# Optimization experiments

Measured on AMD Instinct MI355X. Metric: run time of the kernel, lower is better.

The kernel has to match this reference:

```python
import jax, jax.numpy as jnp
import numpy as np

B, S, H, F, E, TOP_K = 2, 2048, 1024, 2048, 8, 2


def setup_inputs() -> dict:
    key = jax.random.key(0)
    ks = jax.random.split(key, 5)
    scale_h = 1.0 / np.sqrt(H)
    scale_f = 1.0 / np.sqrt(F)
    return {
        "hidden_states": jax.random.normal(ks[0], (B, S, H), jnp.float32),
        "gate_w": jax.random.normal(ks[1], (H, E), jnp.float32) * scale_h,
        "w_up": jax.random.normal(ks[2], (E, H, F), jnp.float32) * scale_h,
        "w_gate": jax.random.normal(ks[3], (E, H, F), jnp.float32) * scale_h,
        "w_down": jax.random.normal(ks[4], (E, F, H), jnp.float32) * scale_f,
    }


def reference(hidden_states, gate_w, w_up, w_gate, w_down):
    b, s, h = hidden_states.shape
    x = hidden_states.reshape(-1, h)                      # [T, H]
    T = x.shape[0]

    # Router: softmax then top-k then renormalize (as in the module)
    router_logits = x @ gate_w                            # [T, E]
    probs = jax.nn.softmax(router_logits, axis=-1)
    routing_weights, selected_experts = jax.lax.top_k(probs, TOP_K)  # [T, K]
    routing_weights = routing_weights / jnp.sum(routing_weights, axis=-1, keepdims=True)
    routing_weights = routing_weights.astype(x.dtype)

    # Per-token combine weight for each expert (sum over k where selected == e).
    # Equals the masked where/+ accumulation in the original (zero where unselected).
    combine = jnp.zeros((T, E), x.dtype).at[
        jnp.arange(T)[:, None], selected_experts
    ].add(routing_weights)                                # [T, E]

    # Dense expert compute on ALL tokens for every expert (faithful to original,
    # where each device runs its expert on the full token set, then psum).
    up = jnp.einsum("th,ehf->etf", x, w_up)               # [E, T, F]
    gate = jnp.einsum("th,ehf->etf", x, w_gate)           # [E, T, F]
    inner = jax.nn.silu(up) * gate                        # note: silu on up_proj, as in source
    expert_out = jnp.einsum("etf,efh->eth", inner, w_down)  # [E, T, H]

    # Weighted combine == psum over expert axis of masked/weighted outputs.
    y = jnp.einsum("te,eth->th", combine, expert_out)     # [T, H]
    return y.reshape(b, s, h)
```

## Files before the change

### kernel.cpp

```cpp
#include <hip/hip_runtime.h>
#include <hip/hip_bf16.h>

typedef __bf16 bf16x8 __attribute__((ext_vector_type(8)));
typedef float f32x4 __attribute__((ext_vector_type(4)));

#define T_TOK 4096
#define H_DIM 1024
#define F_DIM 2048
#define NEXP 8
#define TOTROWS 8192
#define MAXTILES 80

__device__ inline unsigned short f2b(float f) {
    unsigned int u = __float_as_uint(f);
    unsigned int r = (u + 0x7fffu + ((u >> 16) & 1u)) >> 16;
    return (unsigned short)r;
}

__device__ inline void gload16(const void* g, void* l) {
    __builtin_amdgcn_global_load_lds(
        (const __attribute__((address_space(1))) unsigned int*)g,
        (__attribute__((address_space(3))) unsigned int*)l,
        16, 0, 0);
}

__global__ __launch_bounds__(256) void router_kernel(const float* __restrict__ x,
                                                     const float* __restrict__ gw,
                                                     int* __restrict__ sel, float* __restrict__ selw) {
    int t = blockIdx.x * 4 + (threadIdx.x >> 6);
    int lane = threadIdx.x & 63;
    float acc[8] = {0.f,0.f,0.f,0.f,0.f,0.f,0.f,0.f};
    const float* xr = x + (size_t)t * H_DIM;
    for (int h = lane; h < H_DIM; h += 64) {
        float xv = xr[h];
        const float4* g = (const float4*)(gw + h * 8);
        float4 g0 = g[0], g1 = g[1];
        acc[0] += xv * g0.x; acc[1] += xv * g0.y; acc[2] += xv * g0.z; acc[3] += xv * g0.w;
        acc[4] += xv * g1.x; acc[5] += xv * g1.y; acc[6] += xv * g1.z; acc[7] += xv * g1.w;
    }
#pragma unroll
    for (int off = 32; off >= 1; off >>= 1)
#pragma unroll
        for (int e = 0; e < 8; ++e)
            acc[e] += __shfl_down(acc[e], off);
    if (lane == 0) {
        float mx = acc[0];
#pragma unroll
        for (int e = 1; e < 8; ++e) mx = fmaxf(mx, acc[e]);
        float p[8]; float s = 0.f;
#pragma unroll
        for (int e = 0; e < 8; ++e) { p[e] = expf(acc[e] - mx); s += p[e]; }
        float inv_s = 1.f / s;
#pragma unroll
        for (int e = 0; e < 8; ++e) p[e] *= inv_s;
        int e1 = 0; float p1 = p[0];
#pragma unroll
        for (int e = 1; e < 8; ++e) if (p[e] > p1) { p1 = p[e]; e1 = e; }
        int e2 = -1; float p2 = -1.f;
#pragma unroll
        for (int e = 0; e < 8; ++e) { if (e == e1) continue; if (p[e] > p2) { p2 = p[e]; e2 = e; } }
        float inv = 1.f / (p1 + p2);
        sel[t * 2 + 0] = e1; sel[t * 2 + 1] = e2;
        selw[t * 2 + 0] = p1 * inv; selw[t * 2 + 1] = p2 * inv;
    }
}

__global__ __launch_bounds__(256) void scan_kernel(const int* __restrict__ sel,
                                                   int* __restrict__ cnt, int* __restrict__ off,
                                                   int* __restrict__ fill,
                                                   int* __restrict__ tileExp, int* __restrict__ tileM0) {
    __shared__ int h[NEXP];
    int tid = threadIdx.x;
    if (tid < NEXP) h[tid] = 0;
    __syncthreads();
    for (int i = tid; i < TOTROWS; i += 256) atomicAdd(&h[sel[i]], 1);
    __syncthreads();
    if (tid == 0) {
        int o = 0;
        for (int e = 0; e < NEXP; ++e) { cnt[e] = h[e]; off[e] = o; o += h[e]; fill[e] = 0; }
        int nt = 0;
        for (int e = 0; e < NEXP; ++e)
            for (int m0 = 0; m0 < h[e]; m0 += 128) { tileExp[nt] = e; tileM0[nt] = m0; nt++; }
        for (int i = nt; i < MAXTILES; ++i) { tileExp[i] = -1; tileM0[i] = 0; }
    }
}

__global__ __launch_bounds__(256) void scatgath_kernel(const int* __restrict__ sel,
                                                       const float* __restrict__ selw,
                                                       const int* __restrict__ off,
                                                       int* __restrict__ fill,
                                                       float* __restrict__ rowWgt,
                                                       int* __restrict__ tokRow,
                                                       const float* __restrict__ x,
                                                       unsigned short* __restrict__ Xg) {
    __shared__ int rs[2];
    int t = blockIdx.x;
    int tid = threadIdx.x;
    if (tid == 0) {
#pragma unroll
        for (int k = 0; k < 2; ++k) {
            int e = sel[t * 2 + k];
            int slot = atomicAdd(&fill[e], 1);
            int r = off[e] + slot;
            rowWgt[r] = selw[t * 2 + k];
            tokRow[t * 2 + k] = r;
            rs[k] = r;
        }
    }
    __syncthreads();
    int r1 = rs[0], r2 = rs[1];
    float4 v = ((const float4*)(x + (size_t)t * H_DIM))[tid];
    ushort4 o;
    o.x = f2b(v.x); o.y = f2b(v.y); o.z = f2b(v.z); o.w = f2b(v.w);
    ((ushort4*)(Xg + (size_t)r1 * H_DIM))[tid] = o;
    ((ushort4*)(Xg + (size_t)r2 * H_DIM))[tid] = o;
}

__global__ __launch_bounds__(256) void transpose_cvt_kernel(
        const float* __restrict__ w_up, const float* __restrict__ w_gate,
        const float* __restrict__ w_down,
        unsigned short* __restrict__ wTu, unsigned short* __restrict__ wTg,
        unsigned short* __restrict__ wTd) {
    __shared__ unsigned short lt[64 * 68];
    int z = blockIdx.z;
    int e = blockIdx.y;
    const float* src; unsigned short* dst; int R, C, tr, tc;
    if (z == 0)      { src = w_up;   dst = wTu; R = H_DIM; C = F_DIM; }
    else if (z == 1) { src = w_gate; dst = wTg; R = H_DIM; C = F_DIM; }
    else             { src = w_down; dst = wTd; R = F_DIM; C = H_DIM; }
    if (R == H_DIM) { tc = blockIdx.x & 31; tr = blockIdx.x >> 5; }
    else            { tc = blockIdx.x & 15; tr = blockIdx.x >> 4; }
    const float* s = src + (size_t)e * H_DIM * F_DIM;
    unsigned short* d = dst + (size_t)e * H_DIM * F_DIM;
    int r0 = tr * 64, c0 = tc * 64;
    int tid = threadIdx.x;
    int fc = tid & 15, row = tid >> 4;
#pragma unroll
    for (int i = 0; i < 4; ++i) {
        int r = row + i * 16;
        float4 v = *(const float4*)(s + (size_t)(r0 + r) * C + c0 + fc * 4);
        lt[(fc * 4 + 0) * 68 + r] = f2b(v.x);
        lt[(fc * 4 + 1) * 68 + r] = f2b(v.y);
        lt[(fc * 4 + 2) * 68 + r] = f2b(v.z);
        lt[(fc * 4 + 3) * 68 + r] = f2b(v.w);
    }
    __syncthreads();
    int ch = tid & 7, cc = tid >> 3;
#pragma unroll
    for (int i = 0; i < 2; ++i) {
        int c = cc + i * 32;
        uint2 lo = *(const uint2*)&lt[c * 68 + ch * 8];
        uint2 hi = *(const uint2*)&lt[c * 68 + ch * 8 + 4];
        uint4 o = make_uint4(lo.x, lo.y, hi.x, hi.y);
        *(uint4*)(d + (size_t)(c0 + c) * R + r0 + ch * 8) = o;
    }
}

__global__ __launch_bounds__(256, 2) void gemm_upgate_kernel(
        const unsigned short* __restrict__ Xg,
        const unsigned short* __restrict__ wTu,
        const unsigned short* __restrict__ wTg,
        unsigned short* __restrict__ inner,
        const int* __restrict__ tileExp, const int* __restrict__ tileM0,
        const int* __restrict__ off, const int* __restrict__ cnt) {
    __shared__ __align__(16) unsigned short la[128 * 64];
    __shared__ __align__(16) unsigned short lbu[128 * 64];
    __shared__ __align__(16) unsigned short lbg[128 * 64];
    int bt = blockIdx.y;
    int e = tileExp[bt];
    if (e < 0) return;
    int m0 = tileM0[bt];
    int r0 = off[e] + m0;
    int valid = cnt[e] - m0;
    int f0 = blockIdx.x * 128;
    const unsigned short* aB = Xg + (size_t)r0 * H_DIM;
    const unsigned short* bu = wTu + (size_t)e * F_DIM * H_DIM + (size_t)f0 * H_DIM;
    const unsigned short* bg = wTg + (size_t)e * F_DIM * H_DIM + (size_t)f0 * H_DIM;
    int tid = threadIdx.x;
    int lane = tid & 63, wid = tid >> 6;
    int wm = wid >> 1, wn = wid & 1;
    int l16 = lane & 15, quad = lane >> 4;

    int srcOff[4];
#pragma unroll
    for (int it = 0; it < 4; ++it) {
        int chunk = it * 256 + tid;
        int row = chunk >> 3;
        srcOff[it] = row * H_DIM + (((chunk & 7) ^ (row & 7)) << 3);
    }
    f32x4 accU[4][4], accG[4][4];
#pragma unroll
    for (int i = 0; i < 4; ++i)
#pragma unroll
        for (int j = 0; j < 4; ++j) { accU[i][j] = (f32x4)0.f; accG[i][j] = (f32x4)0.f; }

    for (int k0 = 0; k0 < H_DIM; k0 += 64) {
        __syncthreads();
#pragma unroll
        for (int it = 0; it < 4; ++it) {
            int lbase = it * 2048 + wid * 512;
            gload16(aB + srcOff[it] + k0, &la[lbase]);
            gload16(bu + srcOff[it] + k0, &lbu[lbase]);
            gload16(bg + srcOff[it] + k0, &lbg[lbase]);
        }
        __syncthreads();
#pragma unroll
        for (int h = 0; h < 2; ++h) {
            bf16x8 af[4], bfu[4], bfg[4];
#pragma unroll
            for (int i = 0; i < 4; ++i) {
                int lr = wm * 64 + i * 16 + l16;
                af[i] = *(const bf16x8*)&la[lr * 64 + ((((h * 4 + quad) ^ (lr & 7))) << 3)];
            }
#pragma unroll
            for (int j = 0; j < 4; ++j) {
                int lr = wn * 64 + j * 16 + l16;
                int p = lr * 64 + ((((h * 4 + quad) ^ (lr & 7))) << 3);
                bfu[j] = *(const bf16x8*)&lbu[p];
                bfg[j] = *(const bf16x8*)&lbg[p];
            }
#pragma unroll
            for (int i = 0; i < 4; ++i)
#pragma unroll
                for (int j = 0; j < 4; ++j) {
                    accU[i][j] = __builtin_amdgcn_mfma_f32_16x16x32_bf16(af[i], bfu[j], accU[i][j], 0, 0, 0);
                    accG[i][j] = __builtin_amdgcn_mfma_f32_16x16x32_bf16(af[i], bfg[j], accG[i][j], 0, 0, 0);
                }
        }
    }
#pragma unroll
    for (int i = 0; i < 4; ++i) {
#pragma unroll
        for (int rr = 0; rr < 4; ++rr) {
            int ml = wm * 64 + i * 16 + quad * 4 + rr;
            if (ml >= valid) continue;
            size_t base = (size_t)(r0 + ml) * F_DIM + f0;
#pragma unroll
            for (int j = 0; j < 4; ++j) {
                float u = accU[i][j][rr];
                float g = accG[i][j][rr];
                float v = u / (1.f + expf(-u)) * g;
                inner[base + wn * 64 + j * 16 + l16] = f2b(v);
            }
        }
    }
}

__global__ __launch_bounds__(256, 2) void gemm_down_kernel(
        const unsigned short* __restrict__ inner,
        const unsigned short* __restrict__ wTd,
        float* __restrict__ part,
        const int* __restrict__ tileExp, const int* __restrict__ tileM0,
        const int* __restrict__ off, const int* __restrict__ cnt,
        const float* __restrict__ rowWgt) {
    __shared__ __align__(16) unsigned short la[128 * 64];
    __shared__ __align__(16) unsigned short lb[128 * 64];
    int bt = blockIdx.y;
    int e = tileExp[bt];
    if (e < 0) return;
    int m0 = tileM0[bt];
    int r0 = off[e] + m0;
    int valid = cnt[e] - m0;
    int h0 = blockIdx.x * 128;
    const unsigned short* aB = inner + (size_t)r0 * F_DIM;
    const unsigned short* bp = wTd + (size_t)e * H_DIM * F_DIM + (size_t)h0 * F_DIM;
    int tid = threadIdx.x;
    int lane = tid & 63, wid = tid >> 6;
    int wm = wid >> 1, wn = wid & 1;
    int l16 = lane & 15, quad = lane >> 4;

    int srcOff[4];
#pragma unroll
    for (int it = 0; it < 4; ++it) {
        int chunk = it * 256 + tid;
        int row = chunk >> 3;
        srcOff[it] = row * F_DIM + (((chunk & 7) ^ (row & 7)) << 3);
    }
    f32x4 acc[4][4];
#pragma unroll
    for (int i = 0; i < 4; ++i)
#pragma unroll
        for (int j = 0; j < 4; ++j) acc[i][j] = (f32x4)0.f;

    for (int k0 = 0; k0 < F_DIM; k0 += 64) {
        __syncthreads();
#pragma unroll
        for (int it = 0; it < 4; ++it) {
            int lbase = it * 2048 + wid * 512;
            gload16(aB + srcOff[it] + k0, &la[lbase]);
            gload16(bp + srcOff[it] + k0, &lb[lbase]);
        }
        __syncthreads();
#pragma unroll
        for (int h = 0; h < 2; ++h) {
            bf16x8 af[4], bf[4];
#pragma unroll
            for (int i = 0; i < 4; ++i) {
                int lr = wm * 64 + i * 16 + l16;
                af[i] = *(const bf16x8*)&la[lr * 64 + ((((h * 4 + quad) ^ (lr & 7))) << 3)];
            }
#pragma unroll
            for (int j = 0; j < 4; ++j) {
                int lr = wn * 64 + j * 16 + l16;
                bf[j] = *(const bf16x8*)&lb[lr * 64 + ((((h * 4 + quad) ^ (lr & 7))) << 3)];
            }
#pragma unroll
            for (int i = 0; i < 4; ++i)
#pragma unroll
                for (int j = 0; j < 4; ++j)
                    acc[i][j] = __builtin_amdgcn_mfma_f32_16x16x32_bf16(af[i], bf[j], acc[i][j], 0, 0, 0);
        }
    }
#pragma unroll
    for (int i = 0; i < 4; ++i) {
#pragma unroll
        for (int rr = 0; rr < 4; ++rr) {
            int ml = wm * 64 + i * 16 + quad * 4 + rr;
            if (ml >= valid) continue;
            int gr = r0 + ml;
            float w = rowWgt[gr];
            float* orow = part + (size_t)gr * H_DIM + h0;
#pragma unroll
            for (int j = 0; j < 4; ++j)
                orow[wn * 64 + j * 16 + l16] = w * acc[i][j][rr];
        }
    }
}

__global__ __launch_bounds__(256) void combine_kernel(const float* __restrict__ part,
                                                      const int* __restrict__ tokRow,
                                                      float* __restrict__ out) {
    int t = blockIdx.x;
    int r1 = tokRow[t * 2 + 0], r2 = tokRow[t * 2 + 1];
    int i = threadIdx.x;
    float4 a = ((const float4*)(part + (size_t)r1 * H_DIM))[i];
    float4 b = ((const float4*)(part + (size_t)r2 * H_DIM))[i];
    float4 o;
    o.x = a.x + b.x; o.y = a.y + b.y; o.z = a.z + b.z; o.w = a.w + b.w;
    ((float4*)(out + (size_t)t * H_DIM))[i] = o;
}

extern "C" void kernel_launch(void* const* d_in, const int* in_sizes, int n_in,
                              void* d_out, int out_size, void* d_ws, size_t ws_size,
                              hipStream_t stream) {
    const float* x      = (const float*)d_in[0];
    const float* gw     = (const float*)d_in[1];
    const float* w_up   = (const float*)d_in[2];
    const float* w_gate = (const float*)d_in[3];
    const float* w_down = (const float*)d_in[4];
    float* out = (float*)d_out;

    char* ws = (char*)d_ws;
    size_t o = 0;
    unsigned short* wTu = (unsigned short*)(ws + o); o += (size_t)NEXP * F_DIM * H_DIM * 2;
    unsigned short* wTg = (unsigned short*)(ws + o); o += (size_t)NEXP * F_DIM * H_DIM * 2;
    unsigned short* wTd = (unsigned short*)(ws + o); o += (size_t)NEXP * H_DIM * F_DIM * 2;
    unsigned short* Xg  = (unsigned short*)(ws + o); o += (size_t)TOTROWS * H_DIM * 2;
    unsigned short* inner = (unsigned short*)(ws + o); o += (size_t)TOTROWS * F_DIM * 2;
    o += 1024 * 1024;
    float* rowWgt = (float*)(ws + o); o += TOTROWS * 4;
    int*   tokRow = (int*)(ws + o);   o += T_TOK * 2 * 4;
    int*   sel    = (int*)(ws + o);   o += T_TOK * 2 * 4;
    float* selw   = (float*)(ws + o); o += T_TOK * 2 * 4;
    int*   cnt    = (int*)(ws + o);   o += 8 * 4;
    int*   fill   = (int*)(ws + o);   o += 8 * 4;
    int*   off_   = (int*)(ws + o);   o += 8 * 4;
    int*   tileExp = (int*)(ws + o);  o += MAXTILES * 4;
    int*   tileM0  = (int*)(ws + o);  o += MAXTILES * 4;
    float* part = (float*)wTu;

    router_kernel<<<T_TOK / 4, 256, 0, stream>>>(x, gw, sel, selw);
    scan_kernel<<<1, 256, 0, stream>>>(sel, cnt, off_, fill, tileExp, tileM0);
    scatgath_kernel<<<T_TOK, 256, 0, stream>>>(sel, selw, off_, fill, rowWgt, tokRow, x, Xg);
    transpose_cvt_kernel<<<dim3(512, NEXP, 3), 256, 0, stream>>>(w_up, w_gate, w_down, wTu, wTg, wTd);
    gemm_upgate_kernel<<<dim3(F_DIM / 128, 72), 256, 0, stream>>>(Xg, wTu, wTg, inner, tileExp, tileM0, off_, cnt);
    gemm_down_kernel<<<dim3(H_DIM / 128, 72), 256, 0, stream>>>(inner, wTd, part, tileExp, tileM0, off_, cnt, rowWgt);
    combine_kernel<<<T_TOK, 256, 0, stream>>>(part, tokRow, out);
}
```

Measured before the change: 507.7 us.

## Triple-buffer both expert GEMMs with explicit waitcnt pipelining and 256-row up-gate tiles

Both expert GEMMs move from a load-then-compute loop with two syncthreads per step to a 3-stage LDS ring over 32-wide K slices. Explicit vmcnt/lgkmcnt waits, sched barriers and setprio overlap global-to-LDS loads with MFMA work. The up/gate kernel now uses 512 threads and 256-row token tiles from a new tile list, which halves how often each weight tile is reloaded. SiLU switches to a fast exp and rcp. The trade-off is more LDS and register pressure, and the hand-unrolled pipeline tails must match the K trip counts exactly.

```diff
diff --git a/kernel.cpp b/kernel.cpp
--- a/kernel.cpp
+++ b/kernel.cpp
@@ -10,6 +10,7 @@
 #define NEXP 8
 #define TOTROWS 8192
 #define MAXTILES 80
+#define UPT 40
 
 __device__ inline unsigned short f2b(float f) {
     unsigned int u = __float_as_uint(f);
@@ -22,6 +23,17 @@
         (const __attribute__((address_space(1))) unsigned int*)g,
         (__attribute__((address_space(3))) unsigned int*)l,
         16, 0, 0);
+}
+
+__device__ inline int swz_src(int p, int LD) {
+    int sr = p >> 3, s = p & 7;
+    int qq = s ^ (sr & 7);
+    int r = 2 * sr + (qq >> 2);
+    int q = qq & 3;
+    return r * LD + q * 8;
+}
+__device__ inline int swz_frag(int lr, int quad) {
+    return (lr >> 1) * 64 + (((quad | ((lr & 1) << 2)) ^ ((lr >> 1) & 7)) << 3);
 }
 
 __global__ __launch_bounds__(256) void router_kernel(const float* __restrict__ x,
@@ -68,7 +80,8 @@
 __global__ __launch_bounds__(256) void scan_kernel(const int* __restrict__ sel,
                                                    int* __restrict__ cnt, int* __restrict__ off,
                                                    int* __restrict__ fill,
-                                                   int* __restrict__ tileExp, int* __restrict__ tileM0) {
+                                                   int* __restrict__ tileExp, int* __restrict__ tileM0,
+                                                   int* __restrict__ tileExpU, int* __restrict__ tileM0U) {
     __shared__ int h[NEXP];
     int tid = threadIdx.x;
     if (tid < NEXP) h[tid] = 0;
@@ -82,6 +95,10 @@
         for (int e = 0; e < NEXP; ++e)
             for (int m0 = 0; m0 < h[e]; m0 += 128) { tileExp[nt] = e; tileM0[nt] = m0; nt++; }
         for (int i = nt; i < MAXTILES; ++i) { tileExp[i] = -1; tileM0[i] = 0; }
+        int nu = 0;
+        for (int e = 0; e < NEXP; ++e)
+            for (int m0 = 0; m0 < h[e]; m0 += 256) { tileExpU[nu] = e; tileM0U[nu] = m0; nu++; }
+        for (int i = nu; i < UPT; ++i) { tileExpU[i] = -1; tileM0U[i] = 0; }
     }
 }
 
@@ -156,78 +173,106 @@
     }
 }
 
-__global__ __launch_bounds__(256, 2) void gemm_upgate_kernel(
+#define UPG_TILE(VN, B, NB, K2, DOST) do {                                        \
+    asm volatile("s_waitcnt vmcnt(" #VN ")" ::: "memory");                        \
+    __builtin_amdgcn_s_barrier();                                                 \
+    __builtin_amdgcn_sched_barrier(0);                                            \
+    bf16x8 af_[4], bb_[4];                                                        \
+    _Pragma("unroll") for (int x_ = 0; x_ < 4; ++x_)                              \
+        af_[x_] = *(const bf16x8*)&la[B][aIdx[x_]];                               \
+    _Pragma("unroll") for (int x_ = 0; x_ < 4; ++x_)                              \
+        bb_[x_] = *(const bf16x8*)&lbu[B][bIdx[x_]];                              \
+    if (DOST) { gload16(aB + sA0 + (K2), &la[NB][dA0]);                           \
+                gload16(aB + sA1 + (K2), &la[NB][dA1]); }                         \
+    __builtin_amdgcn_s_barrier();                                                 \
+    asm volatile("s_waitcnt lgkmcnt(0)" ::: "memory");                            \
+    __builtin_amdgcn_sched_barrier(0);                                            \
+    __builtin_amdgcn_s_setprio(1);                                                \
+    _Pragma("unroll") for (int i_ = 0; i_ < 4; ++i_)                              \
+        _Pragma("unroll") for (int j_ = 0; j_ < 4; ++j_)                          \
+            accU[i_][j_] = __builtin_amdgcn_mfma_f32_16x16x32_bf16(af_[i_], bb_[j_], accU[i_][j_], 0, 0, 0); \
+    __builtin_amdgcn_s_setprio(0);                                                \
+    __builtin_amdgcn_sched_barrier(0);                                            \
+    __builtin_amdgcn_s_barrier();                                                 \
+    _Pragma("unroll") for (int x_ = 0; x_ < 4; ++x_)                              \
+        bb_[x_] = *(const bf16x8*)&lbg[B][bIdx[x_]];                              \
+    if (DOST) { gload16(buW + sB + (K2), &lbu[NB][dB]);                           \
+                gload16(bgW + sB + (K2), &lbg[NB][dB]); }                         \
+    __builtin_amdgcn_s_barrier();                                                 \
+    asm volatile("s_waitcnt lgkmcnt(0)" ::: "memory");                            \
+    __builtin_amdgcn_sched_barrier(0);                                            \
+    __builtin_amdgcn_s_setprio(1);                                                \
+    _Pragma("unroll") for (int i_ = 0; i_ < 4; ++i_)                              \
+        _Pragma("unroll") for (int j_ = 0; j_ < 4; ++j_)                          \
+            accG[i_][j_] = __builtin_amdgcn_mfma_f32_16x16x32_bf16(af_[i_], bb_[j_], accG[i_][j_], 0, 0, 0); \
+    __builtin_amdgcn_s_setprio(0);                                                \
+    __builtin_amdgcn_sched_barrier(0);                                            \
+    __builtin_amdgcn_s_barrier();                                                 \
+} while (0)
+
+#define UPG_STAGE_ALL(K2, NB) do {                                                \
+    gload16(aB + sA0 + (K2), &la[NB][dA0]);                                       \
+    gload16(aB + sA1 + (K2), &la[NB][dA1]);                                       \
+    gload16(buW + sB + (K2), &lbu[NB][dB]);                                       \
+    gload16(bgW + sB + (K2), &lbg[NB][dB]);                                       \
+} while (0)
+
+__global__ __launch_bounds__(512, 2) void gemm_upgate_kernel(
         const unsigned short* __restrict__ Xg,
         const unsigned short* __restrict__ wTu,
         const unsigned short* __restrict__ wTg,
         unsigned short* __restrict__ inner,
-        const int* __restrict__ tileExp, const int* __restrict__ tileM0,
+        const int* __restrict__ tileExpU, const int* __restrict__ tileM0U,
         const int* __restrict__ off, const int* __restrict__ cnt) {
-    __shared__ __align__(16) unsigned short la[128 * 64];
-    __shared__ __align__(16) unsigned short lbu[128 * 64];
-    __shared__ __align__(16) unsigned short lbg[128 * 64];
+    __shared__ __align__(16) unsigned short la[3][8192];
+    __shared__ __align__(16) unsigned short lbu[3][4096];
+    __shared__ __align__(16) unsigned short lbg[3][4096];
     int bt = blockIdx.y;
-    int e = tileExp[bt];
+    int e = tileExpU[bt];
     if (e < 0) return;
-    int m0 = tileM0[bt];
+    int m0 = tileM0U[bt];
     int r0 = off[e] + m0;
     int valid = cnt[e] - m0;
     int f0 = blockIdx.x * 128;
-    const unsigned short* aB = Xg + (size_t)r0 * H_DIM;
-    const unsigned short* bu = wTu + (size_t)e * F_DIM * H_DIM + (size_t)f0 * H_DIM;
-    const unsigned short* bg = wTg + (size_t)e * F_DIM * H_DIM + (size_t)f0 * H_DIM;
+    const unsigned short* aB  = Xg + (size_t)r0 * H_DIM;
+    const unsigned short* buW = wTu + (size_t)e * F_DIM * H_DIM + (size_t)f0 * H_DIM;
+    const unsigned short* bgW = wTg + (size_t)e * F_DIM * H_DIM + (size_t)f0 * H_DIM;
     int tid = threadIdx.x;
     int lane = tid & 63, wid = tid >> 6;
     int wm = wid >> 1, wn = wid & 1;
     int l16 = lane & 15, quad = lane >> 4;
 
-    int srcOff[4];
-#pragma unroll
-    for (int it = 0; it < 4; ++it) {
-        int chunk = it * 256 + tid;
-        int row = chunk >> 3;
-        srcOff[it] = row * H_DIM + (((chunk & 7) ^ (row & 7)) << 3);
-    }
+    int sA0 = swz_src(tid, H_DIM);
+    int sA1 = swz_src(512 + tid, H_DIM);
+    int sB  = swz_src(tid, H_DIM);
+    int dA0 = wid * 512;
+    int dA1 = 4096 + wid * 512;
+    int dB  = wid * 512;
+
+    int aIdx[4], bIdx[4];
+#pragma unroll
+    for (int i = 0; i < 4; ++i) aIdx[i] = swz_frag(wm * 64 + i * 16 + l16, quad);
+#pragma unroll
+    for (int j = 0; j < 4; ++j) bIdx[j] = swz_frag(wn * 64 + j * 16 + l16, quad);
+
     f32x4 accU[4][4], accG[4][4];
 #pragma unroll
     for (int i = 0; i < 4; ++i)
 #pragma unroll
         for (int j = 0; j < 4; ++j) { accU[i][j] = (f32x4)0.f; accG[i][j] = (f32x4)0.f; }
 
-    for (int k0 = 0; k0 < H_DIM; k0 += 64) {
-        __syncthreads();
-#pragma unroll
-        for (int it = 0; it < 4; ++it) {
-            int lbase = it * 2048 + wid * 512;
-            gload16(aB + srcOff[it] + k0, &la[lbase]);
-            gload16(bu + srcOff[it] + k0, &lbu[lbase]);
-            gload16(bg + srcOff[it] + k0, &lbg[lbase]);
-        }
-        __syncthreads();
-#pragma unroll
-        for (int h = 0; h < 2; ++h) {
-            bf16x8 af[4], bfu[4], bfg[4];
-#pragma unroll
-            for (int i = 0; i < 4; ++i) {
-                int lr = wm * 64 + i * 16 + l16;
-                af[i] = *(const bf16x8*)&la[lr * 64 + ((((h * 4 + quad) ^ (lr & 7))) << 3)];
-            }
-#pragma unroll
-            for (int j = 0; j < 4; ++j) {
-                int lr = wn * 64 + j * 16 + l16;
-                int p = lr * 64 + ((((h * 4 + quad) ^ (lr & 7))) << 3);
-                bfu[j] = *(const bf16x8*)&lbu[p];
-                bfg[j] = *(const bf16x8*)&lbg[p];
-            }
-#pragma unroll
-            for (int i = 0; i < 4; ++i)
-#pragma unroll
-                for (int j = 0; j < 4; ++j) {
-                    accU[i][j] = __builtin_amdgcn_mfma_f32_16x16x32_bf16(af[i], bfu[j], accU[i][j], 0, 0, 0);
-                    accG[i][j] = __builtin_amdgcn_mfma_f32_16x16x32_bf16(af[i], bfg[j], accG[i][j], 0, 0, 0);
-                }
-        }
-    }
+    UPG_STAGE_ALL(0, 0);
+    UPG_STAGE_ALL(32, 1);
+
+    for (int t = 0; t < 30; t += 3) {
+        int k2 = (t + 2) * 32;
+        UPG_TILE(4, 0, 2, k2, 1);
+        UPG_TILE(4, 1, 0, k2 + 32, 1);
+        UPG_TILE(4, 2, 1, k2 + 64, 1);
+    }
+    UPG_TILE(4, 0, 0, 0, 0);
+    UPG_TILE(0, 1, 0, 0, 0);
+
 #pragma unroll
     for (int i = 0; i < 4; ++i) {
 #pragma unroll
@@ -239,22 +284,54 @@
             for (int j = 0; j < 4; ++j) {
                 float u = accU[i][j][rr];
                 float g = accG[i][j][rr];
-                float v = u / (1.f + expf(-u)) * g;
+                float v = u * __builtin_amdgcn_rcpf(1.f + __expf(-u)) * g;
                 inner[base + wn * 64 + j * 16 + l16] = f2b(v);
             }
         }
     }
 }
 
-__global__ __launch_bounds__(256, 2) void gemm_down_kernel(
+#define DWN_TILE(VN, B, NB, K2, DOST) do {                                        \
+    asm volatile("s_waitcnt vmcnt(" #VN ")" ::: "memory");                        \
+    __builtin_amdgcn_s_barrier();                                                 \
+    __builtin_amdgcn_sched_barrier(0);                                            \
+    bf16x8 af_[4], bw_[4];                                                        \
+    _Pragma("unroll") for (int x_ = 0; x_ < 4; ++x_)                              \
+        af_[x_] = *(const bf16x8*)&la[B][aIdx[x_]];                               \
+    _Pragma("unroll") for (int x_ = 0; x_ < 4; ++x_)                              \
+        bw_[x_] = *(const bf16x8*)&lb[B][bIdx[x_]];                               \
+    if (DOST) { gload16(aB + s0 + (K2), &la[NB][d0]);                             \
+                gload16(aB + s1 + (K2), &la[NB][d1]);                             \
+                gload16(bp + s0 + (K2), &lb[NB][d0]);                             \
+                gload16(bp + s1 + (K2), &lb[NB][d1]); }                           \
+    __builtin_amdgcn_s_barrier();                                                 \
+    asm volatile("s_waitcnt lgkmcnt(0)" ::: "memory");                            \
+    __builtin_amdgcn_sched_barrier(0);                                            \
+    __builtin_amdgcn_s_setprio(1);                                                \
+    _Pragma("unroll") for (int i_ = 0; i_ < 4; ++i_)                              \
+        _Pragma("unroll") for (int j_ = 0; j_ < 4; ++j_)                          \
+            acc[i_][j_] = __builtin_amdgcn_mfma_f32_16x16x32_bf16(af_[i_], bw_[j_], acc[i_][j_], 0, 0, 0); \
+    __builtin_amdgcn_s_setprio(0);                                                \
+    __builtin_amdgcn_sched_barrier(0);                                            \
+    __builtin_amdgcn_s_barrier();                                                 \
+} while (0)
+
+#define DWN_STAGE_ALL(K2, NB) do {                                                \
+    gload16(aB + s0 + (K2), &la[NB][d0]);                                         \
+    gload16(aB + s1 + (K2), &la[NB][d1]);                                         \
+    gload16(bp + s0 + (K2), &lb[NB][d0]);                                         \
+    gload16(bp + s1 + (K2), &lb[NB][d1]);                                         \
+} while (0)
+
+__global__ __launch_bounds__(256, 3) void gemm_down_kernel(
         const unsigned short* __restrict__ inner,
         const unsigned short* __restrict__ wTd,
         float* __restrict__ part,
         const int* __restrict__ tileExp, const int* __restrict__ tileM0,
         const int* __restrict__ off, const int* __restrict__ cnt,
         const float* __restrict__ rowWgt) {
-    __shared__ __align__(16) unsigned short la[128 * 64];
-    __shared__ __align__(16) unsigned short lb[128 * 64];
+    __shared__ __align__(16) unsigned short la[3][4096];
+    __shared__ __align__(16) unsigned short lb[3][4096];
     int bt = blockIdx.y;
     int e = tileExp[bt];
     if (e < 0) return;
@@ -269,48 +346,37 @@
     int wm = wid >> 1, wn = wid & 1;
     int l16 = lane & 15, quad = lane >> 4;
 
-    int srcOff[4];
-#pragma unroll
-    for (int it = 0; it < 4; ++it) {
-        int chunk = it * 256 + tid;
-        int row = chunk >> 3;
-        srcOff[it] = row * F_DIM + (((chunk & 7) ^ (row & 7)) << 3);
-    }
+    int s0 = swz_src(tid, F_DIM);
+    int s1 = swz_src(256 + tid, F_DIM);
+    int d0 = wid * 512;
+    int d1 = 2048 + wid * 512;
+
+    int aIdx[4], bIdx[4];
+#pragma unroll
+    for (int i = 0; i < 4; ++i) aIdx[i] = swz_frag(wm * 64 + i * 16 + l16, quad);
+#pragma unroll
+    for (int j = 0; j < 4; ++j) bIdx[j] = swz_frag(wn * 64 + j * 16 + l16, quad);
+
     f32x4 acc[4][4];
 #pragma unroll
     for (int i = 0; i < 4; ++i)
 #pragma unroll
         for (int j = 0; j < 4; ++j) acc[i][j] = (f32x4)0.f;
 
-    for (int k0 = 0; k0 < F_DIM; k0 += 64) {
-        __syncthreads();
-#pragma unroll
-        for (int it = 0; it < 4; ++it) {
-            int lbase = it * 2048 + wid * 512;
-            gload16(aB + srcOff[it] + k0, &la[lbase]);
-            gload16(bp + srcOff[it] + k0, &lb[lbase]);
-        }
-        __syncthreads();
-#pragma unroll
-        for (int h = 0; h < 2; ++h) {
-            bf16x8 af[4], bf[4];
-#pragma unroll
-            for (int i = 0; i < 4; ++i) {
-                int lr = wm * 64 + i * 16 + l16;
-                af[i] = *(const bf16x8*)&la[lr * 64 + ((((h * 4 + quad) ^ (lr & 7))) << 3)];
-            }
-#pragma unroll
-            for (int j = 0; j < 4; ++j) {
-                int lr = wn * 64 + j * 16 + l16;
-                bf[j] = *(const bf16x8*)&lb[lr * 64 + ((((h * 4 + quad) ^ (lr & 7))) << 3)];
-            }
-#pragma unroll
-            for (int i = 0; i < 4; ++i)
-#pragma unroll
-                for (int j = 0; j < 4; ++j)
-                    acc[i][j] = __builtin_amdgcn_mfma_f32_16x16x32_bf16(af[i], bf[j], acc[i][j], 0, 0, 0);
-        }
-    }
+    DWN_STAGE_ALL(0, 0);
+    DWN_STAGE_ALL(32, 1);
+
+    for (int t = 0; t < 60; t += 3) {
+        int k2 = (t + 2) * 32;
+        DWN_TILE(4, 0, 2, k2, 1);
+        DWN_TILE(4, 1, 0, k2 + 32, 1);
+        DWN_TILE(4, 2, 1, k2 + 64, 1);
+    }
+    DWN_TILE(4, 0, 2, 62 * 32, 1);
+    DWN_TILE(4, 1, 0, 63 * 32, 1);
+    DWN_TILE(4, 2, 0, 0, 0);
+    DWN_TILE(0, 0, 0, 0, 0);
+
 #pragma unroll
     for (int i = 0; i < 4; ++i) {
 #pragma unroll
@@ -357,7 +423,7 @@
     unsigned short* wTd = (unsigned short*)(ws + o); o += (size_t)NEXP * H_DIM * F_DIM * 2;
     unsigned short* Xg  = (unsigned short*)(ws + o); o += (size_t)TOTROWS * H_DIM * 2;
     unsigned short* inner = (unsigned short*)(ws + o); o += (size_t)TOTROWS * F_DIM * 2;
-    o += 1024 * 1024;
+    o += 2 * 1024 * 1024;
     float* rowWgt = (float*)(ws + o); o += TOTROWS * 4;
     int*   tokRow = (int*)(ws + o);   o += T_TOK * 2 * 4;
     int*   sel    = (int*)(ws + o);   o += T_TOK * 2 * 4;
@@ -367,13 +433,15 @@
     int*   off_   = (int*)(ws + o);   o += 8 * 4;
     int*   tileExp = (int*)(ws + o);  o += MAXTILES * 4;
     int*   tileM0  = (int*)(ws + o);  o += MAXTILES * 4;
+    int*   tileExpU = (int*)(ws + o); o += UPT * 4;
+    int*   tileM0U  = (int*)(ws + o); o += UPT * 4;
     float* part = (float*)wTu;
 
     router_kernel<<<T_TOK / 4, 256, 0, stream>>>(x, gw, sel, selw);
-    scan_kernel<<<1, 256, 0, stream>>>(sel, cnt, off_, fill, tileExp, tileM0);
+    scan_kernel<<<1, 256, 0, stream>>>(sel, cnt, off_, fill, tileExp, tileM0, tileExpU, tileM0U);
     scatgath_kernel<<<T_TOK, 256, 0, stream>>>(sel, selw, off_, fill, rowWgt, tokRow, x, Xg);
     transpose_cvt_kernel<<<dim3(512, NEXP, 3), 256, 0, stream>>>(w_up, w_gate, w_down, wTu, wTg, wTd);
-    gemm_upgate_kernel<<<dim3(F_DIM / 128, 72), 256, 0, stream>>>(Xg, wTu, wTg, inner, tileExp, tileM0, off_, cnt);
+    gemm_upgate_kernel<<<dim3(F_DIM / 128, UPT), 512, 0, stream>>>(Xg, wTu, wTg, inner, tileExpU, tileM0U, off_, cnt);
     gemm_down_kernel<<<dim3(H_DIM / 128, 72), 256, 0, stream>>>(inner, wTd, part, tileExp, tileM0, off_, cnt, rowWgt);
     combine_kernel<<<T_TOK, 256, 0, stream>>>(part, tokRow, out);
 }
```

New measurement: 515.8 us. Within noise of the previous version (+1.6%).

## Double-buffer LDS in expert GEMMs with register-staged prefetch and BK=32

Applied to the files above, without the earlier changes.

Both expert GEMM kernels drop direct global-to-LDS loads with two barriers per 64-wide K step. They now use a two-stage LDS ping-pong at K step 32: global loads go into registers two steps ahead, are written into the idle buffer, and the step ends with one barrier. MFMA sections are wrapped in raised wave priority, and the down GEMM's launch bounds ask for 3 blocks per CU. SiLU switches to fast exp and a hardware reciprocal, and the workspace padding grows. The goal is to hide global-load latency behind MFMA work and halve barrier count per K element, at the cost of more registers and a smaller swizzle width.

```diff
diff --git a/kernel.cpp b/kernel.cpp
--- a/kernel.cpp
+++ b/kernel.cpp
@@ -15,13 +15,6 @@
     unsigned int u = __float_as_uint(f);
     unsigned int r = (u + 0x7fffu + ((u >> 16) & 1u)) >> 16;
     return (unsigned short)r;
-}
-
-__device__ inline void gload16(const void* g, void* l) {
-    __builtin_amdgcn_global_load_lds(
-        (const __attribute__((address_space(1))) unsigned int*)g,
-        (__attribute__((address_space(3))) unsigned int*)l,
-        16, 0, 0);
 }
 
 __global__ __launch_bounds__(256) void router_kernel(const float* __restrict__ x,
@@ -163,9 +156,9 @@
         unsigned short* __restrict__ inner,
         const int* __restrict__ tileExp, const int* __restrict__ tileM0,
         const int* __restrict__ off, const int* __restrict__ cnt) {
-    __shared__ __align__(16) unsigned short la[128 * 64];
-    __shared__ __align__(16) unsigned short lbu[128 * 64];
-    __shared__ __align__(16) unsigned short lbg[128 * 64];
+    __shared__ __align__(16) unsigned short la[2][4096];
+    __shared__ __align__(16) unsigned short lbu[2][4096];
+    __shared__ __align__(16) unsigned short lbg[2][4096];
     int bt = blockIdx.y;
     int e = tileExp[bt];
     if (e < 0) return;
@@ -173,61 +166,92 @@
     int r0 = off[e] + m0;
     int valid = cnt[e] - m0;
     int f0 = blockIdx.x * 128;
-    const unsigned short* aB = Xg + (size_t)r0 * H_DIM;
-    const unsigned short* bu = wTu + (size_t)e * F_DIM * H_DIM + (size_t)f0 * H_DIM;
-    const unsigned short* bg = wTg + (size_t)e * F_DIM * H_DIM + (size_t)f0 * H_DIM;
+    const unsigned short* aB  = Xg + (size_t)r0 * H_DIM;
+    const unsigned short* buW = wTu + (size_t)e * F_DIM * H_DIM + (size_t)f0 * H_DIM;
+    const unsigned short* bgW = wTg + (size_t)e * F_DIM * H_DIM + (size_t)f0 * H_DIM;
     int tid = threadIdx.x;
     int lane = tid & 63, wid = tid >> 6;
     int wm = wid >> 1, wn = wid & 1;
     int l16 = lane & 15, quad = lane >> 4;
 
-    int srcOff[4];
-#pragma unroll
-    for (int it = 0; it < 4; ++it) {
-        int chunk = it * 256 + tid;
-        int row = chunk >> 3;
-        srcOff[it] = row * H_DIM + (((chunk & 7) ^ (row & 7)) << 3);
-    }
+    int rA0 = tid >> 2, rA1 = rA0 + 64;
+    int s0 = rA0 * H_DIM + (tid & 3) * 8;
+    int s1 = rA1 * H_DIM + (tid & 3) * 8;
+    int d0 = rA0 * 32 + (((tid & 3) ^ (rA0 & 3)) << 3);
+    int d1 = rA1 * 32 + (((tid & 3) ^ (rA1 & 3)) << 3);
+
+    int aIdx[4], bIdx[4];
+#pragma unroll
+    for (int i = 0; i < 4; ++i) {
+        int lr = wm * 64 + i * 16 + l16;
+        aIdx[i] = lr * 32 + ((quad ^ (lr & 3)) << 3);
+    }
+#pragma unroll
+    for (int j = 0; j < 4; ++j) {
+        int lr = wn * 64 + j * 16 + l16;
+        bIdx[j] = lr * 32 + ((quad ^ (lr & 3)) << 3);
+    }
+
     f32x4 accU[4][4], accG[4][4];
 #pragma unroll
     for (int i = 0; i < 4; ++i)
 #pragma unroll
         for (int j = 0; j < 4; ++j) { accU[i][j] = (f32x4)0.f; accG[i][j] = (f32x4)0.f; }
 
-    for (int k0 = 0; k0 < H_DIM; k0 += 64) {
-        __syncthreads();
-#pragma unroll
-        for (int it = 0; it < 4; ++it) {
-            int lbase = it * 2048 + wid * 512;
-            gload16(aB + srcOff[it] + k0, &la[lbase]);
-            gload16(bu + srcOff[it] + k0, &lbu[lbase]);
-            gload16(bg + srcOff[it] + k0, &lbg[lbase]);
+    uint4 va0, va1, vu0, vu1, vg0, vg1;
+
+#define UPG_LOAD(K0) do {                                        \
+    va0 = *(const uint4*)(aB + s0 + (K0));                       \
+    va1 = *(const uint4*)(aB + s1 + (K0));                       \
+    vu0 = *(const uint4*)(buW + s0 + (K0));                      \
+    vu1 = *(const uint4*)(buW + s1 + (K0));                      \
+    vg0 = *(const uint4*)(bgW + s0 + (K0));                      \
+    vg1 = *(const uint4*)(bgW + s1 + (K0));                      \
+} while (0)
+#define UPG_WRITE(NB) do {                                       \
+    *(uint4*)&la[NB][d0]  = va0;  *(uint4*)&la[NB][d1]  = va1;   \
+    *(uint4*)&lbu[NB][d0] = vu0;  *(uint4*)&lbu[NB][d1] = vu1;   \
+    *(uint4*)&lbg[NB][d0] = vg0;  *(uint4*)&lbg[NB][d1] = vg1;   \
+} while (0)
+
+    UPG_LOAD(0);
+    UPG_WRITE(0);
+    UPG_LOAD(32);
+    asm volatile("s_waitcnt lgkmcnt(0)" ::: "memory");
+    __builtin_amdgcn_s_barrier();
+    __builtin_amdgcn_sched_barrier(0);
+
+    for (int t = 0; t < 32; ++t) {
+        int cur = t & 1, nxt = cur ^ 1;
+        const unsigned short* lac = la[cur];
+        const unsigned short* luc = lbu[cur];
+        const unsigned short* lgc = lbg[cur];
+        bf16x8 af[4], bu[4], bg[4];
+#pragma unroll
+        for (int i = 0; i < 4; ++i) af[i] = *(const bf16x8*)(lac + aIdx[i]);
+#pragma unroll
+        for (int j = 0; j < 4; ++j) {
+            bu[j] = *(const bf16x8*)(luc + bIdx[j]);
+            bg[j] = *(const bf16x8*)(lgc + bIdx[j]);
         }
-        __syncthreads();
-#pragma unroll
-        for (int h = 0; h < 2; ++h) {
-            bf16x8 af[4], bfu[4], bfg[4];
-#pragma unroll
-            for (int i = 0; i < 4; ++i) {
-                int lr = wm * 64 + i * 16 + l16;
-                af[i] = *(const bf16x8*)&la[lr * 64 + ((((h * 4 + quad) ^ (lr & 7))) << 3)];
+        if (t < 31) UPG_WRITE(nxt);
+        if (t < 30) UPG_LOAD((t + 2) * 32);
+        __builtin_amdgcn_s_setprio(1);
+#pragma unroll
+        for (int i = 0; i < 4; ++i)
+#pragma unroll
+            for (int j = 0; j < 4; ++j) {
+                accU[i][j] = __builtin_amdgcn_mfma_f32_16x16x32_bf16(af[i], bu[j], accU[i][j], 0, 0, 0);
+                accG[i][j] = __builtin_amdgcn_mfma_f32_16x16x32_bf16(af[i], bg[j], accG[i][j], 0, 0, 0);
             }
-#pragma unroll
-            for (int j = 0; j < 4; ++j) {
-                int lr = wn * 64 + j * 16 + l16;
-                int p = lr * 64 + ((((h * 4 + quad) ^ (lr & 7))) << 3);
-                bfu[j] = *(const bf16x8*)&lbu[p];
-                bfg[j] = *(const bf16x8*)&lbg[p];
-            }
-#pragma unroll
-            for (int i = 0; i < 4; ++i)
-#pragma unroll
-                for (int j = 0; j < 4; ++j) {
-                    accU[i][j] = __builtin_amdgcn_mfma_f32_16x16x32_bf16(af[i], bfu[j], accU[i][j], 0, 0, 0);
-                    accG[i][j] = __builtin_amdgcn_mfma_f32_16x16x32_bf16(af[i], bfg[j], accG[i][j], 0, 0, 0);
-                }
-        }
-    }
+        __builtin_amdgcn_s_setprio(0);
+        asm volatile("s_waitcnt lgkmcnt(0)" ::: "memory");
+        __builtin_amdgcn_s_barrier();
+        __builtin_amdgcn_sched_barrier(0);
+    }
+#undef UPG_LOAD
+#undef UPG_WRITE
+
 #pragma unroll
     for (int i = 0; i < 4; ++i) {
 #pragma unroll
@@ -239,22 +263,22 @@
             for (int j = 0; j < 4; ++j) {
                 float u = accU[i][j][rr];
                 float g = accG[i][j][rr];
-                float v = u / (1.f + expf(-u)) * g;
+                float v = u * __builtin_amdgcn_rcpf(1.f + __expf(-u)) * g;
                 inner[base + wn * 64 + j * 16 + l16] = f2b(v);
             }
         }
     }
 }
 
-__global__ __launch_bounds__(256, 2) void gemm_down_kernel(
+__global__ __launch_bounds__(256, 3) void gemm_down_kernel(
         const unsigned short* __restrict__ inner,
         const unsigned short* __restrict__ wTd,
         float* __restrict__ part,
         const int* __restrict__ tileExp, const int* __restrict__ tileM0,
         const int* __restrict__ off, const int* __restrict__ cnt,
         const float* __restrict__ rowWgt) {
-    __shared__ __align__(16) unsigned short la[128 * 64];
-    __shared__ __align__(16) unsigned short lb[128 * 64];
+    __shared__ __align__(16) unsigned short la[2][4096];
+    __shared__ __align__(16) unsigned short lb[2][4096];
     int bt = blockIdx.y;
     int e = tileExp[bt];
     if (e < 0) return;
@@ -269,48 +293,75 @@
     int wm = wid >> 1, wn = wid & 1;
     int l16 = lane & 15, quad = lane >> 4;
 
-    int srcOff[4];
-#pragma unroll
-    for (int it = 0; it < 4; ++it) {
-        int chunk = it * 256 + tid;
-        int row = chunk >> 3;
-        srcOff[it] = row * F_DIM + (((chunk & 7) ^ (row & 7)) << 3);
-    }
+    int rA0 = tid >> 2, rA1 = rA0 + 64;
+    int s0 = rA0 * F_DIM + (tid & 3) * 8;
+    int s1 = rA1 * F_DIM + (tid & 3) * 8;
+    int d0 = rA0 * 32 + (((tid & 3) ^ (rA0 & 3)) << 3);
+    int d1 = rA1 * 32 + (((tid & 3) ^ (rA1 & 3)) << 3);
+
+    int aIdx[4], bIdx[4];
+#pragma unroll
+    for (int i = 0; i < 4; ++i) {
+        int lr = wm * 64 + i * 16 + l16;
+        aIdx[i] = lr * 32 + ((quad ^ (lr & 3)) << 3);
+    }
+#pragma unroll
+    for (int j = 0; j < 4; ++j) {
+        int lr = wn * 64 + j * 16 + l16;
+        bIdx[j] = lr * 32 + ((quad ^ (lr & 3)) << 3);
+    }
+
     f32x4 acc[4][4];
 #pragma unroll
     for (int i = 0; i < 4; ++i)
 #pragma unroll
         for (int j = 0; j < 4; ++j) acc[i][j] = (f32x4)0.f;
 
-    for (int k0 = 0; k0 < F_DIM; k0 += 64) {
-        __syncthreads();
-#pragma unroll
-        for (int it = 0; it < 4; ++it) {
-            int lbase = it * 2048 + wid * 512;
-            gload16(aB + srcOff[it] + k0, &la[lbase]);
-            gload16(bp + srcOff[it] + k0, &lb[lbase]);
-        }
-        __syncthreads();
-#pragma unroll
-        for (int h = 0; h < 2; ++h) {
-            bf16x8 af[4], bf[4];
-#pragma unroll
-            for (int i = 0; i < 4; ++i) {
-                int lr = wm * 64 + i * 16 + l16;
-                af[i] = *(const bf16x8*)&la[lr * 64 + ((((h * 4 + quad) ^ (lr & 7))) << 3)];
-            }
-#pragma unroll
-            for (int j = 0; j < 4; ++j) {
-                int lr = wn * 64 + j * 16 + l16;
-                bf[j] = *(const bf16x8*)&lb[lr * 64 + ((((h * 4 + quad) ^ (lr & 7))) << 3)];
-            }
-#pragma unroll
-            for (int i = 0; i < 4; ++i)
-#pragma unroll
-                for (int j = 0; j < 4; ++j)
-                    acc[i][j] = __builtin_amdgcn_mfma_f32_16x16x32_bf16(af[i], bf[j], acc[i][j], 0, 0, 0);
-        }
-    }
+    uint4 va0, va1, vb0, vb1;
+
+#define DWN_LOAD(K0) do {                                        \
+    va0 = *(const uint4*)(aB + s0 + (K0));                       \
+    va1 = *(const uint4*)(aB + s1 + (K0));                       \
+    vb0 = *(const uint4*)(bp + s0 + (K0));                       \
+    vb1 = *(const uint4*)(bp + s1 + (K0));                       \
+} while (0)
+#define DWN_WRITE(NB) do {                                       \
+    *(uint4*)&la[NB][d0] = va0;  *(uint4*)&la[NB][d1] = va1;     \
+    *(uint4*)&lb[NB][d0] = vb0;  *(uint4*)&lb[NB][d1] = vb1;     \
+} while (0)
+
+    DWN_LOAD(0);
+    DWN_WRITE(0);
+    DWN_LOAD(32);
+    asm volatile("s_waitcnt lgkmcnt(0)" ::: "memory");
+    __builtin_amdgcn_s_barrier();
+    __builtin_amdgcn_sched_barrier(0);
+
+    for (int t = 0; t < 64; ++t) {
+        int cur = t & 1, nxt = cur ^ 1;
+        const unsigned short* lac = la[cur];
+        const unsigned short* lbc = lb[cur];
+        bf16x8 af[4], bw[4];
+#pragma unroll
+        for (int i = 0; i < 4; ++i) af[i] = *(const bf16x8*)(lac + aIdx[i]);
+#pragma unroll
+        for (int j = 0; j < 4; ++j) bw[j] = *(const bf16x8*)(lbc + bIdx[j]);
+        if (t < 63) DWN_WRITE(nxt);
+        if (t < 62) DWN_LOAD((t + 2) * 32);
+        __builtin_amdgcn_s_setprio(1);
+#pragma unroll
+        for (int i = 0; i < 4; ++i)
+#pragma unroll
+            for (int j = 0; j < 4; ++j)
+                acc[i][j] = __builtin_amdgcn_mfma_f32_16x16x32_bf16(af[i], bw[j], acc[i][j], 0, 0, 0);
+        __builtin_amdgcn_s_setprio(0);
+        asm volatile("s_waitcnt lgkmcnt(0)" ::: "memory");
+        __builtin_amdgcn_s_barrier();
+        __builtin_amdgcn_sched_barrier(0);
+    }
+#undef DWN_LOAD
+#undef DWN_WRITE
+
 #pragma unroll
     for (int i = 0; i < 4; ++i) {
 #pragma unroll
@@ -357,7 +408,7 @@
     unsigned short* wTd = (unsigned short*)(ws + o); o += (size_t)NEXP * H_DIM * F_DIM * 2;
     unsigned short* Xg  = (unsigned short*)(ws + o); o += (size_t)TOTROWS * H_DIM * 2;
     unsigned short* inner = (unsigned short*)(ws + o); o += (size_t)TOTROWS * F_DIM * 2;
-    o += 1024 * 1024;
+    o += 2 * 1024 * 1024;
     float* rowWgt = (float*)(ws + o); o += TOTROWS * 4;
     int*   tokRow = (int*)(ws + o);   o += T_TOK * 2 * 4;
     int*   sel    = (int*)(ws + o);   o += T_TOK * 2 * 4;
```

New measurement: 502.0 us. Within noise of the previous version (-1.1%).
